# Performance work log

Measured on AMD Instinct MI355X. Metric: run time of the kernel, lower is better.

## Reference

```python
import jax, jax.numpy as jnp
import numpy as np

ALPHA = 1000.0


def setup_inputs() -> dict:
    key = jax.random.key(0)
    ks = jax.random.split(key, 5)
    B, D_in, K = 8192, 2048, 256  # K = n_clusters = embed_dim (square cluster_reps)
    x = jax.random.normal(ks[0], (B, D_in), dtype=jnp.float32)
    W_enc = jax.random.normal(ks[1], (D_in, K), dtype=jnp.float32) * (1.0 / np.sqrt(D_in))
    b_enc = jnp.zeros((K,), dtype=jnp.float32)
    W_dec = jax.random.normal(ks[2], (K, D_in), dtype=jnp.float32) * (1.0 / np.sqrt(K))
    b_dec = jnp.zeros((D_in,), dtype=jnp.float32)
    cluster_reps = jax.random.normal(ks[3], (K, K), dtype=jnp.float32)
    return {"x": x, "W_enc": W_enc, "b_enc": b_enc, "W_dec": W_dec,
            "b_dec": b_dec, "cluster_reps": cluster_reps}


def reference(x, W_enc, b_enc, W_dec, b_dec, cluster_reps):
    # Autoencoder (linear MLP stand-in for the injected module)
    emb = x @ W_enc + b_enc                    # [B, K]
    reconstruction = emb @ W_dec + b_dec       # [B, D_in]

    # Squared Euclidean distance to each cluster rep, in GEMM form: [B, K]
    # dist[b, k] = ||emb_b||^2 - 2 emb_b . c_k + ||c_k||^2
    dist = (jnp.sum(emb * emb, axis=1, keepdims=True)
            - 2.0 * (emb @ cluster_reps.T)
            + jnp.sum(cluster_reps * cluster_reps, axis=1)[None, :])

    stack_dist = dist.T                        # [K, B] (matches torch.stack over clusters)
    min_dist = jnp.min(stack_dist, axis=0)     # [B]
    stack_exp = jnp.exp(-ALPHA * (stack_dist - min_dist[None, :]))  # stable softmin
    softmax = stack_exp / jnp.sum(stack_exp, axis=0, keepdims=True)
    weighted_dist = stack_dist * softmax       # [K, B]
    return weighted_dist, reconstruction
```

## Files before the change

### kernel.cpp

```cpp
#include <hip/hip_runtime.h>

#define ALPHA_F 1000.0f

typedef _Float16 half8 __attribute__((ext_vector_type(8)));
typedef float floatx4 __attribute__((ext_vector_type(4)));

__device__ __forceinline__ void gload_lds16(const void* g, void* l) {
    __builtin_amdgcn_global_load_lds(
        (const __attribute__((address_space(1))) unsigned int*)g,
        (__attribute__((address_space(3))) unsigned int*)l, 16, 0, 0);
}

__global__ __launch_bounds__(256) void prep(
    const float* __restrict__ W_enc, const float* __restrict__ W_dec,
    const float* __restrict__ creps,
    _Float16* __restrict__ Wh, _Float16* __restrict__ Wl,
    _Float16* __restrict__ Wdh,
    _Float16* __restrict__ Ch, _Float16* __restrict__ Cl,
    float* __restrict__ cnorm)
{
    const int bid = blockIdx.x;
    if (bid < 256) {
        const int q = bid * 256 + threadIdx.x;
        const int n = q & 255, k8 = q >> 8;
        const int k = k8 * 8;
        half8 h, l;
        #pragma unroll
        for (int i = 0; i < 8; ++i) {
            const float v = W_enc[(size_t)(k + i) * 256 + n] * 256.0f;
            const _Float16 hi = (_Float16)v;
            h[i] = hi;
            l[i] = (_Float16)(v - (float)hi);
        }
        const int kc = k >> 5, nt = n >> 4;
        const int lane = (n & 15) | ((k8 & 3) << 4);
        const size_t idx = (size_t)((kc * 16 + nt) * 64 + lane) * 8;
        *(half8*)(Wh + idx) = h;
        *(half8*)(Wl + idx) = l;
    } else if (bid < 512) {
        const int q = (bid - 256) * 256 + threadIdx.x;
        const int n = q & 2047, k8 = q >> 11;
        const int k = k8 * 8;
        half8 h;
        #pragma unroll
        for (int i = 0; i < 8; ++i) h[i] = (_Float16)W_dec[(size_t)(k + i) * 2048 + n];
        const int kc = k8 >> 2, nt = n >> 4;
        const int lane = (n & 15) | ((k8 & 3) << 4);
        *(half8*)(Wdh + (size_t)((kc * 128 + nt) * 64 + lane) * 8) = h;
    } else if (bid < 544) {
        const int q = (bid - 512) * 256 + threadIdx.x;
        const int n = q & 255, j8 = q >> 8;
        const int j = j8 * 8;
        half8 h, l;
        #pragma unroll
        for (int i = 0; i < 8; ++i) {
            const float v = creps[(size_t)n * 256 + j + i];
            const _Float16 hi = (_Float16)v;
            h[i] = hi;
            l[i] = (_Float16)((v - (float)hi) * 2048.0f);
        }
        const int jc = j >> 5, nt = n >> 4;
        const int lane = (n & 15) | ((j8 & 3) << 4);
        const size_t idx = (size_t)((jc * 16 + nt) * 64 + lane) * 8;
        *(half8*)(Ch + idx) = h;
        *(half8*)(Cl + idx) = l;
    } else {
        const int wid = threadIdx.x >> 6, lane = threadIdx.x & 63;
        const int row = (bid - 544) * 4 + wid;
        const float4 v = *(const float4*)(creps + (size_t)row * 256 + lane * 4);
        float s = v.x * v.x + v.y * v.y + v.z * v.z + v.w * v.w;
        #pragma unroll
        for (int off = 32; off >= 1; off >>= 1) s += __shfl_xor(s, off, 64);
        if (lane == 0) cnorm[row] = s;
    }
}

__global__ __launch_bounds__(256) void emb_gemm(
    const float* __restrict__ x, const _Float16* __restrict__ Wh,
    const _Float16* __restrict__ Wl, float* __restrict__ P)
{
    __shared__ _Float16 Ah[4 * 64 * 8], Al[4 * 64 * 8];
    __shared__ _Float16 Bh[16 * 64 * 8], Bl[16 * 64 * 8];
    const int t = threadIdx.x, lane = t & 63, w = t >> 6;
    const int kk = blockIdx.x;
    const int mb = blockIdx.y;
    const int m0 = mb * 64;

    const int am = t >> 2, q = t & 3;
    _Float16* AhW = Ah + (((am >> 4) * 64) + ((am & 15) | (q << 4))) * 8;
    _Float16* AlW = Al + (((am >> 4) * 64) + ((am & 15) | (q << 4))) * 8;
    const float* xP = x + (size_t)(m0 + am) * 2048 + kk * 512 + q * 8;

    floatx4 acc[4][4] = {};

    for (int it = 0; it < 16; ++it) {
        const float4 v0 = *(const float4*)(xP + it * 32);
        const float4 v1 = *(const float4*)(xP + it * 32 + 4);
        const int kc = kk * 16 + it;
        __syncthreads();
        const _Float16* bh_src = Wh + (size_t)kc * 16 * 512;
        const _Float16* bl_src = Wl + (size_t)kc * 16 * 512;
        #pragma unroll
        for (int i = 0; i < 4; ++i) {
            const int c = w * 4 + i;
            gload_lds16(bh_src + (size_t)c * 512 + lane * 8, Bh + c * 512);
            gload_lds16(bl_src + (size_t)c * 512 + lane * 8, Bl + c * 512);
        }
        half8 h8, l8;
        {
            const float vv[8] = {v0.x, v0.y, v0.z, v0.w, v1.x, v1.y, v1.z, v1.w};
            #pragma unroll
            for (int i = 0; i < 8; ++i) {
                const _Float16 hi = (_Float16)vv[i];
                h8[i] = hi;
                l8[i] = (_Float16)(vv[i] - (float)hi);
            }
        }
        *(half8*)AhW = h8;
        *(half8*)AlW = l8;
        __syncthreads();

        half8 ah[4], al[4], bh[4], bl[4];
        #pragma unroll
        for (int s = 0; s < 4; ++s) {
            ah[s] = *(const half8*)(Ah + (s * 64 + lane) * 8);
            al[s] = *(const half8*)(Al + (s * 64 + lane) * 8);
        }
        #pragma unroll
        for (int ni = 0; ni < 4; ++ni) {
            bh[ni] = *(const half8*)(Bh + ((w * 4 + ni) * 64 + lane) * 8);
            bl[ni] = *(const half8*)(Bl + ((w * 4 + ni) * 64 + lane) * 8);
        }
        #pragma unroll
        for (int mi = 0; mi < 4; ++mi) {
            #pragma unroll
            for (int ni = 0; ni < 4; ++ni) {
                acc[mi][ni] = __builtin_amdgcn_mfma_f32_16x16x32_f16(ah[mi], bl[ni], acc[mi][ni], 0, 0, 0);
                acc[mi][ni] = __builtin_amdgcn_mfma_f32_16x16x32_f16(al[mi], bh[ni], acc[mi][ni], 0, 0, 0);
                acc[mi][ni] = __builtin_amdgcn_mfma_f32_16x16x32_f16(ah[mi], bh[ni], acc[mi][ni], 0, 0, 0);
            }
        }
    }

    float* Pk = P + (size_t)kk * 2097152;
    #pragma unroll
    for (int mi = 0; mi < 4; ++mi) {
        #pragma unroll
        for (int ni = 0; ni < 4; ++ni) {
            const int col = w * 64 + ni * 16 + (lane & 15);
            const int rowBase = m0 + mi * 16 + (lane >> 4) * 4;
            #pragma unroll
            for (int r = 0; r < 4; ++r)
                Pk[(size_t)(rowBase + r) * 256 + col] = acc[mi][ni][r];
        }
    }
}

__global__ __launch_bounds__(256) void fin_dist(
    const float* __restrict__ P, const float* __restrict__ b_enc,
    const _Float16* __restrict__ ch, const _Float16* __restrict__ cl,
    const float* __restrict__ cnorm,
    _Float16* __restrict__ ehg, float* __restrict__ out)
{
    __shared__ float femb[32 * 257];
    __shared__ float ENORM[32], MINV[32], SUMV[32];
    const int t = threadIdx.x, lane = t & 63, w = t >> 6;
    const int b0 = blockIdx.x * 32;
    const int row = t >> 3, c8 = t & 7;

    {
        const float* p0 = P + (size_t)(b0 + row) * 256 + c8 * 32;
        float4 v[8];
        #pragma unroll
        for (int i = 0; i < 8; ++i) v[i] = *(const float4*)(p0 + i * 4);
        #pragma unroll
        for (int kk = 1; kk < 4; ++kk) {
            const float* pk = p0 + (size_t)kk * 2097152;
            #pragma unroll
            for (int i = 0; i < 8; ++i) {
                const float4 a = *(const float4*)(pk + i * 4);
                v[i].x += a.x; v[i].y += a.y; v[i].z += a.z; v[i].w += a.w;
            }
        }
        const float inv = 1.0f / 256.0f;
        float ssq = 0.0f;
        #pragma unroll
        for (int i = 0; i < 8; ++i) {
            const float4 b = *(const float4*)(b_enc + c8 * 32 + i * 4);
            float4 e;
            e.x = v[i].x * inv + b.x; e.y = v[i].y * inv + b.y;
            e.z = v[i].z * inv + b.z; e.w = v[i].w * inv + b.w;
            femb[row * 257 + c8 * 32 + i * 4 + 0] = e.x;
            femb[row * 257 + c8 * 32 + i * 4 + 1] = e.y;
            femb[row * 257 + c8 * 32 + i * 4 + 2] = e.z;
            femb[row * 257 + c8 * 32 + i * 4 + 3] = e.w;
            ssq += e.x * e.x; ssq += e.y * e.y; ssq += e.z * e.z; ssq += e.w * e.w;
        }
        ssq += __shfl_xor(ssq, 1, 64);
        ssq += __shfl_xor(ssq, 2, 64);
        ssq += __shfl_xor(ssq, 4, 64);
        if (c8 == 0) ENORM[row] = ssq;
    }
    __syncthreads();

    {
        const int grow = b0 + row;
        #pragma unroll
        for (int oo = 0; oo < 4; ++oo) {
            const int q = c8 * 4 + oo;
            const float* src = femb + row * 257 + q * 8;
            half8 h;
            #pragma unroll
            for (int i = 0; i < 8; ++i) h[i] = (_Float16)src[i];
            const size_t idx = (size_t)(((grow >> 4) * 8 + (q >> 2)) * 64
                                        + ((grow & 15) | ((q & 3) << 4))) * 8;
            *(half8*)(ehg + idx) = h;
        }
    }

    floatx4 acc[2][4] = {}, accX[2][4] = {};
    const int arow16 = lane & 15, aoct = lane >> 4;
    for (int kc = 0; kc < 8; ++kc) {
        half8 ah[2], al[2];
        #pragma unroll
        for (int mi = 0; mi < 2; ++mi) {
            const float* fp = femb + (mi * 16 + arow16) * 257 + kc * 32 + aoct * 8;
            #pragma unroll
            for (int j = 0; j < 8; ++j) {
                const float vv = fp[j];
                const _Float16 hi = (_Float16)vv;
                ah[mi][j] = hi;
                al[mi][j] = (_Float16)((vv - (float)hi) * 2048.0f);
            }
        }
        #pragma unroll
        for (int ni = 0; ni < 4; ++ni) {
            const size_t bb = (size_t)((kc * 16 + (w * 4 + ni)) * 64 + lane) * 8;
            const half8 bh = *(const half8*)(ch + bb);
            const half8 bl = *(const half8*)(cl + bb);
            #pragma unroll
            for (int mi = 0; mi < 2; ++mi) {
                acc[mi][ni]  = __builtin_amdgcn_mfma_f32_16x16x32_f16(ah[mi], bh, acc[mi][ni], 0, 0, 0);
                accX[mi][ni] = __builtin_amdgcn_mfma_f32_16x16x32_f16(ah[mi], bl, accX[mi][ni], 0, 0, 0);
                accX[mi][ni] = __builtin_amdgcn_mfma_f32_16x16x32_f16(al[mi], bh, accX[mi][ni], 0, 0, 0);
            }
        }
    }
    __syncthreads();

    float* D = femb;
    const float invs = 1.0f / 2048.0f;
    #pragma unroll
    for (int mi = 0; mi < 2; ++mi) {
        #pragma unroll
        for (int ni = 0; ni < 4; ++ni) {
            const int k = w * 64 + ni * 16 + (lane & 15);
            const float cn = cnorm[k];
            #pragma unroll
            for (int r = 0; r < 4; ++r) {
                const int rl = mi * 16 + (lane >> 4) * 4 + r;
                const float S = acc[mi][ni][r] + accX[mi][ni][r] * invs;
                D[rl * 257 + k] = ENORM[rl] - 2.0f * S + cn;
            }
        }
    }
    __syncthreads();

    #pragma unroll
    for (int rr = 0; rr < 8; ++rr) {
        const int r = w * 8 + rr;
        const float d0 = D[r * 257 + lane +   0];
        const float d1 = D[r * 257 + lane +  64];
        const float d2 = D[r * 257 + lane + 128];
        const float d3 = D[r * 257 + lane + 192];
        float mn = fminf(fminf(d0, d1), fminf(d2, d3));
        #pragma unroll
        for (int off = 32; off >= 1; off >>= 1) mn = fminf(mn, __shfl_xor(mn, off, 64));
        float s = expf(-ALPHA_F * (d0 - mn)) + expf(-ALPHA_F * (d1 - mn))
                + expf(-ALPHA_F * (d2 - mn)) + expf(-ALPHA_F * (d3 - mn));
        #pragma unroll
        for (int off = 32; off >= 1; off >>= 1) s += __shfl_xor(s, off, 64);
        if (lane == 0) { MINV[r] = mn; SUMV[r] = s; }
    }
    __syncthreads();

    const int b = t & 31, kg = t >> 5;
    const float mn = MINV[b], sv = SUMV[b];
    #pragma unroll
    for (int kk = 0; kk < 32; ++kk) {
        const int k = kk * 8 + kg;
        const float dv = D[b * 257 + k];
        out[(size_t)k * 8192 + b0 + b] = dv * expf(-ALPHA_F * (dv - mn)) / sv;
    }
}

__global__ __launch_bounds__(256) void recon_gemm(
    const _Float16* __restrict__ embh, const _Float16* __restrict__ Wdh,
    const float* __restrict__ b_dec, float* __restrict__ out)
{
    __shared__ _Float16 Ah[8 * 64 * 8];
    __shared__ _Float16 Bh[8 * 64 * 8];
    const int t = threadIdx.x, lane = t & 63, w = t >> 6;
    const int wm = w >> 1, wn = w & 1;
    const int nb = blockIdx.x, mb = blockIdx.y;

    floatx4 acc[4][4] = {};

    for (int kc = 0; kc < 8; ++kc) {
        __syncthreads();
        #pragma unroll
        for (int i = 0; i < 2; ++i) {
            const int c = w * 2 + i;
            gload_lds16(embh + (size_t)(((mb * 8 + c) * 8 + kc) * 64 + lane) * 8, Ah + c * 512);
            gload_lds16(Wdh + (size_t)((kc * 128 + nb * 8 + c) * 64 + lane) * 8, Bh + c * 512);
        }
        __syncthreads();
        half8 a[4], b[4];
        #pragma unroll
        for (int mi = 0; mi < 4; ++mi) a[mi] = *(const half8*)(Ah + ((wm * 4 + mi) * 64 + lane) * 8);
        #pragma unroll
        for (int ni = 0; ni < 4; ++ni) b[ni] = *(const half8*)(Bh + ((wn * 4 + ni) * 64 + lane) * 8);
        #pragma unroll
        for (int mi = 0; mi < 4; ++mi)
            #pragma unroll
            for (int ni = 0; ni < 4; ++ni)
                acc[mi][ni] = __builtin_amdgcn_mfma_f32_16x16x32_f16(a[mi], b[ni], acc[mi][ni], 0, 0, 0);
    }

    #pragma unroll
    for (int ni = 0; ni < 4; ++ni) {
        const int col = nb * 128 + (wn * 4 + ni) * 16 + (lane & 15);
        const float bias = b_dec[col];
        #pragma unroll
        for (int mi = 0; mi < 4; ++mi) {
            const int rowBase = mb * 128 + (wm * 4 + mi) * 16 + (lane >> 4) * 4;
            #pragma unroll
            for (int r = 0; r < 4; ++r)
                out[(size_t)(rowBase + r) * 2048 + col] = acc[mi][ni][r] + bias;
        }
    }
}

extern "C" void kernel_launch(void* const* d_in, const int* in_sizes, int n_in,
                              void* d_out, int out_size, void* d_ws, size_t ws_size,
                              hipStream_t stream) {
    const float* x     = (const float*)d_in[0];
    const float* W_enc = (const float*)d_in[1];
    const float* b_enc = (const float*)d_in[2];
    const float* W_dec = (const float*)d_in[3];
    const float* b_dec = (const float*)d_in[4];
    const float* creps = (const float*)d_in[5];

    float* out_w   = (float*)d_out;
    float* out_rec = out_w + (size_t)256 * 8192;
    float* P       = out_rec;

    float*     cnorm = (float*)d_ws;
    _Float16*  embh  = (_Float16*)(cnorm + 256);
    _Float16*  Whf   = embh + (size_t)8192 * 256;
    _Float16*  Wlf   = Whf + (size_t)2048 * 256;
    _Float16*  Wdh   = Wlf + (size_t)2048 * 256;
    _Float16*  crh   = Wdh + (size_t)256 * 2048;
    _Float16*  crl   = crh + (size_t)256 * 256;

    prep<<<608, 256, 0, stream>>>(W_enc, W_dec, creps, Whf, Wlf, Wdh, crh, crl, cnorm);

    emb_gemm<<<dim3(4, 128), 256, 0, stream>>>(x, Whf, Wlf, P);

    fin_dist<<<256, 256, 0, stream>>>(P, b_enc, crh, crl, cnorm, embh, out_w);

    recon_gemm<<<dim3(16, 64), 256, 0, stream>>>(embh, Wdh, b_dec, out_rec);
}
```

Before: 204.3 us.

## Split fused finalize+distance kernel into two kernels with 16-row distance tiles

The fused split-K reduction/distance/softmin kernel is split in two. A finalize kernel reduces the partial sums, adds the bias, and writes the fp32 embedding, its fp16 copy and the row norms to global memory. A separate dist16 kernel runs on 512 blocks of 16 rows and computes the distance GEMM plus the softmin and transposed output. The goal is more blocks and less shared memory per block for better occupancy, at the cost of an extra launch and a round trip of the embedding through global memory.

```diff
diff --git a/kernel.cpp b/kernel.cpp
--- a/kernel.cpp
+++ b/kernel.cpp
@@ -156,119 +156,119 @@
     }
 }
 
-__global__ __launch_bounds__(256) void fin_dist(
+__global__ __launch_bounds__(256) void finalize(
     const float* __restrict__ P, const float* __restrict__ b_enc,
-    const _Float16* __restrict__ ch, const _Float16* __restrict__ cl,
-    const float* __restrict__ cnorm,
-    _Float16* __restrict__ ehg, float* __restrict__ out)
-{
-    __shared__ float femb[32 * 257];
-    __shared__ float ENORM[32], MINV[32], SUMV[32];
-    const int t = threadIdx.x, lane = t & 63, w = t >> 6;
+    _Float16* __restrict__ ehg, float* __restrict__ embf,
+    float* __restrict__ enorm)
+{
+    const int t = threadIdx.x;
     const int b0 = blockIdx.x * 32;
     const int row = t >> 3, c8 = t & 7;
-
-    {
-        const float* p0 = P + (size_t)(b0 + row) * 256 + c8 * 32;
-        float4 v[8];
-        #pragma unroll
-        for (int i = 0; i < 8; ++i) v[i] = *(const float4*)(p0 + i * 4);
-        #pragma unroll
-        for (int kk = 1; kk < 4; ++kk) {
-            const float* pk = p0 + (size_t)kk * 2097152;
-            #pragma unroll
-            for (int i = 0; i < 8; ++i) {
-                const float4 a = *(const float4*)(pk + i * 4);
-                v[i].x += a.x; v[i].y += a.y; v[i].z += a.z; v[i].w += a.w;
-            }
-        }
-        const float inv = 1.0f / 256.0f;
-        float ssq = 0.0f;
+    const int grow = b0 + row;
+
+    const float* p0 = P + (size_t)grow * 256 + c8 * 32;
+    float4 v[8];
+    #pragma unroll
+    for (int i = 0; i < 8; ++i) v[i] = *(const float4*)(p0 + i * 4);
+    #pragma unroll
+    for (int kk = 1; kk < 4; ++kk) {
+        const float* pk = p0 + (size_t)kk * 2097152;
         #pragma unroll
         for (int i = 0; i < 8; ++i) {
-            const float4 b = *(const float4*)(b_enc + c8 * 32 + i * 4);
-            float4 e;
-            e.x = v[i].x * inv + b.x; e.y = v[i].y * inv + b.y;
-            e.z = v[i].z * inv + b.z; e.w = v[i].w * inv + b.w;
-            femb[row * 257 + c8 * 32 + i * 4 + 0] = e.x;
-            femb[row * 257 + c8 * 32 + i * 4 + 1] = e.y;
-            femb[row * 257 + c8 * 32 + i * 4 + 2] = e.z;
-            femb[row * 257 + c8 * 32 + i * 4 + 3] = e.w;
-            ssq += e.x * e.x; ssq += e.y * e.y; ssq += e.z * e.z; ssq += e.w * e.w;
-        }
-        ssq += __shfl_xor(ssq, 1, 64);
-        ssq += __shfl_xor(ssq, 2, 64);
-        ssq += __shfl_xor(ssq, 4, 64);
-        if (c8 == 0) ENORM[row] = ssq;
-    }
-    __syncthreads();
-
-    {
-        const int grow = b0 + row;
-        #pragma unroll
-        for (int oo = 0; oo < 4; ++oo) {
-            const int q = c8 * 4 + oo;
-            const float* src = femb + row * 257 + q * 8;
-            half8 h;
-            #pragma unroll
-            for (int i = 0; i < 8; ++i) h[i] = (_Float16)src[i];
-            const size_t idx = (size_t)(((grow >> 4) * 8 + (q >> 2)) * 64
-                                        + ((grow & 15) | ((q & 3) << 4))) * 8;
-            *(half8*)(ehg + idx) = h;
-        }
-    }
-
-    floatx4 acc[2][4] = {}, accX[2][4] = {};
+            const float4 a = *(const float4*)(pk + i * 4);
+            v[i].x += a.x; v[i].y += a.y; v[i].z += a.z; v[i].w += a.w;
+        }
+    }
+    const float inv = 1.0f / 256.0f;
+    float e[32];
+    float ssq = 0.0f;
+    #pragma unroll
+    for (int i = 0; i < 8; ++i) {
+        const float4 b = *(const float4*)(b_enc + c8 * 32 + i * 4);
+        e[i * 4 + 0] = v[i].x * inv + b.x;
+        e[i * 4 + 1] = v[i].y * inv + b.y;
+        e[i * 4 + 2] = v[i].z * inv + b.z;
+        e[i * 4 + 3] = v[i].w * inv + b.w;
+        ssq += e[i * 4 + 0] * e[i * 4 + 0];
+        ssq += e[i * 4 + 1] * e[i * 4 + 1];
+        ssq += e[i * 4 + 2] * e[i * 4 + 2];
+        ssq += e[i * 4 + 3] * e[i * 4 + 3];
+    }
+    #pragma unroll
+    for (int i = 0; i < 8; ++i) {
+        float4 s4;
+        s4.x = e[i * 4 + 0]; s4.y = e[i * 4 + 1];
+        s4.z = e[i * 4 + 2]; s4.w = e[i * 4 + 3];
+        *(float4*)(embf + (size_t)grow * 256 + c8 * 32 + i * 4) = s4;
+    }
+    #pragma unroll
+    for (int oo = 0; oo < 4; ++oo) {
+        const int q = c8 * 4 + oo;
+        half8 h;
+        #pragma unroll
+        for (int i = 0; i < 8; ++i) h[i] = (_Float16)e[oo * 8 + i];
+        const size_t idx = (size_t)(((grow >> 4) * 8 + (q >> 2)) * 64
+                                    + ((grow & 15) | ((q & 3) << 4))) * 8;
+        *(half8*)(ehg + idx) = h;
+    }
+    ssq += __shfl_xor(ssq, 1, 64);
+    ssq += __shfl_xor(ssq, 2, 64);
+    ssq += __shfl_xor(ssq, 4, 64);
+    if (c8 == 0) enorm[grow] = ssq;
+}
+
+__global__ __launch_bounds__(256) void dist16(
+    const float* __restrict__ embf, const _Float16* __restrict__ ch,
+    const _Float16* __restrict__ cl, const float* __restrict__ enorm,
+    const float* __restrict__ cnorm, float* __restrict__ out)
+{
+    __shared__ float D[16 * 257];
+    __shared__ float MINV[16], SUMV[16];
+    const int t = threadIdx.x, lane = t & 63, w = t >> 6;
+    const int b0 = blockIdx.x * 16;
     const int arow16 = lane & 15, aoct = lane >> 4;
+
+    floatx4 acc[4] = {}, accX[4] = {};
     for (int kc = 0; kc < 8; ++kc) {
-        half8 ah[2], al[2];
-        #pragma unroll
-        for (int mi = 0; mi < 2; ++mi) {
-            const float* fp = femb + (mi * 16 + arow16) * 257 + kc * 32 + aoct * 8;
-            #pragma unroll
-            for (int j = 0; j < 8; ++j) {
-                const float vv = fp[j];
-                const _Float16 hi = (_Float16)vv;
-                ah[mi][j] = hi;
-                al[mi][j] = (_Float16)((vv - (float)hi) * 2048.0f);
-            }
+        const float* fp = embf + (size_t)(b0 + arow16) * 256 + kc * 32 + aoct * 8;
+        const float4 u0 = *(const float4*)(fp);
+        const float4 u1 = *(const float4*)(fp + 4);
+        const float vv[8] = {u0.x, u0.y, u0.z, u0.w, u1.x, u1.y, u1.z, u1.w};
+        half8 ah, al;
+        #pragma unroll
+        for (int j = 0; j < 8; ++j) {
+            const _Float16 hi = (_Float16)vv[j];
+            ah[j] = hi;
+            al[j] = (_Float16)((vv[j] - (float)hi) * 2048.0f);
         }
         #pragma unroll
         for (int ni = 0; ni < 4; ++ni) {
             const size_t bb = (size_t)((kc * 16 + (w * 4 + ni)) * 64 + lane) * 8;
             const half8 bh = *(const half8*)(ch + bb);
             const half8 bl = *(const half8*)(cl + bb);
-            #pragma unroll
-            for (int mi = 0; mi < 2; ++mi) {
-                acc[mi][ni]  = __builtin_amdgcn_mfma_f32_16x16x32_f16(ah[mi], bh, acc[mi][ni], 0, 0, 0);
-                accX[mi][ni] = __builtin_amdgcn_mfma_f32_16x16x32_f16(ah[mi], bl, accX[mi][ni], 0, 0, 0);
-                accX[mi][ni] = __builtin_amdgcn_mfma_f32_16x16x32_f16(al[mi], bh, accX[mi][ni], 0, 0, 0);
-            }
+            acc[ni]  = __builtin_amdgcn_mfma_f32_16x16x32_f16(ah, bh, acc[ni], 0, 0, 0);
+            accX[ni] = __builtin_amdgcn_mfma_f32_16x16x32_f16(ah, bl, accX[ni], 0, 0, 0);
+            accX[ni] = __builtin_amdgcn_mfma_f32_16x16x32_f16(al, bh, accX[ni], 0, 0, 0);
+        }
+    }
+
+    const float invs = 1.0f / 2048.0f;
+    #pragma unroll
+    for (int ni = 0; ni < 4; ++ni) {
+        const int k = w * 64 + ni * 16 + (lane & 15);
+        const float cn = cnorm[k];
+        #pragma unroll
+        for (int r = 0; r < 4; ++r) {
+            const int rl = (lane >> 4) * 4 + r;
+            const float S = acc[ni][r] + accX[ni][r] * invs;
+            D[rl * 257 + k] = enorm[b0 + rl] - 2.0f * S + cn;
         }
     }
     __syncthreads();
 
-    float* D = femb;
-    const float invs = 1.0f / 2048.0f;
-    #pragma unroll
-    for (int mi = 0; mi < 2; ++mi) {
-        #pragma unroll
-        for (int ni = 0; ni < 4; ++ni) {
-            const int k = w * 64 + ni * 16 + (lane & 15);
-            const float cn = cnorm[k];
-            #pragma unroll
-            for (int r = 0; r < 4; ++r) {
-                const int rl = mi * 16 + (lane >> 4) * 4 + r;
-                const float S = acc[mi][ni][r] + accX[mi][ni][r] * invs;
-                D[rl * 257 + k] = ENORM[rl] - 2.0f * S + cn;
-            }
-        }
-    }
-    __syncthreads();
-
-    #pragma unroll
-    for (int rr = 0; rr < 8; ++rr) {
-        const int r = w * 8 + rr;
+    #pragma unroll
+    for (int rr = 0; rr < 4; ++rr) {
+        const int r = w * 4 + rr;
         const float d0 = D[r * 257 + lane +   0];
         const float d1 = D[r * 257 + lane +  64];
         const float d2 = D[r * 257 + lane + 128];
@@ -284,11 +284,11 @@
     }
     __syncthreads();
 
-    const int b = t & 31, kg = t >> 5;
+    const int b = t & 15, kg = t >> 4;
     const float mn = MINV[b], sv = SUMV[b];
     #pragma unroll
-    for (int kk = 0; kk < 32; ++kk) {
-        const int k = kk * 8 + kg;
+    for (int kk = 0; kk < 16; ++kk) {
+        const int k = kk * 16 + kg;
         const float dv = D[b * 257 + k];
         out[(size_t)k * 8192 + b0 + b] = dv * expf(-ALPHA_F * (dv - mn)) / sv;
     }
@@ -362,12 +362,16 @@
     _Float16*  Wdh   = Wlf + (size_t)2048 * 256;
     _Float16*  crh   = Wdh + (size_t)256 * 2048;
     _Float16*  crl   = crh + (size_t)256 * 256;
+    float*     enorm = (float*)(crl + (size_t)256 * 256);
+    float*     embf  = enorm + 8192;
 
     prep<<<608, 256, 0, stream>>>(W_enc, W_dec, creps, Whf, Wlf, Wdh, crh, crl, cnorm);
 
     emb_gemm<<<dim3(4, 128), 256, 0, stream>>>(x, Whf, Wlf, P);
 
-    fin_dist<<<256, 256, 0, stream>>>(P, b_enc, crh, crl, cnorm, embh, out_w);
+    finalize<<<256, 256, 0, stream>>>(P, b_enc, embh, embf, enorm);
+
+    dist16<<<512, 256, 0, stream>>>(embf, crh, crl, enorm, cnorm, out_w);
 
     recon_gemm<<<dim3(16, 64), 256, 0, stream>>>(embh, Wdh, b_dec, out_rec);
 }
```

Result: faster. 199.3 us (-2.4%).
